# Kernel tuning notes

Measured on AMD Instinct MI355X. Metric: run time of the kernel, lower is better.

Reference implementation:

```python
import jax, jax.numpy as jnp
import numpy as np

DIM, HEAD, FFN = 256, 4, 1024
NEG = -1e9


def layer_norm(x, g, b, eps=1e-5):
    mu = jnp.mean(x, axis=-1, keepdims=True)
    var = jnp.mean((x - mu) ** 2, axis=-1, keepdims=True)
    return (x - mu) / jnp.sqrt(var + eps) * g + b


def setup_inputs() -> dict:
    key = jax.random.key(0)
    ks = jax.random.split(key, 10)
    B, T, D = 8, 2048, DIM
    s = 1.0 / np.sqrt(D)
    x = jax.random.normal(ks[0], (B, T, D), dtype=jnp.float32)
    mask = jax.random.randint(ks[1], (B, T), 0, 2).astype(jnp.float32)
    Wqkv = jax.random.uniform(ks[2], (3 * D, D), jnp.float32, -s, s)
    bqkv = jnp.zeros((3 * D,), jnp.float32)
    Wo = jax.random.uniform(ks[3], (D, D), jnp.float32, -s, s)
    bo = jnp.zeros((D,), jnp.float32)
    W1 = jax.random.uniform(ks[4], (FFN, D), jnp.float32, -s, s)
    b1 = jnp.zeros((FFN,), jnp.float32)
    W2 = jax.random.uniform(ks[5], (D, FFN), jnp.float32, -1.0 / np.sqrt(FFN), 1.0 / np.sqrt(FFN))
    b2 = jnp.zeros((D,), jnp.float32)
    g1 = jnp.ones((D,), jnp.float32); be1 = jnp.zeros((D,), jnp.float32)
    g2 = jnp.ones((D,), jnp.float32); be2 = jnp.zeros((D,), jnp.float32)
    return dict(x=x, mask=mask, Wqkv=Wqkv, bqkv=bqkv, Wo=Wo, bo=bo,
                W1=W1, b1=b1, W2=W2, b2=b2, g1=g1, be1=be1, g2=g2, be2=be2)


def _forward(x, mask, Wqkv, bqkv, Wo, bo, W1, b1, W2, b2, g1, be1, g2, be2):
    B, T, D = x.shape
    H = HEAD
    hd = D // H
    # --- MultiheadAttention (explicit, non-flash path, need_weights=True) ---
    qkv = jnp.einsum('btd,ed->bte', x, Wqkv) + bqkv            # (B,T,3D)
    q, k, v = jnp.split(qkv, 3, axis=-1)
    q = q.reshape(B, T, H, hd).transpose(0, 2, 1, 3)           # (B,H,T,hd)
    k = k.reshape(B, T, H, hd).transpose(0, 2, 1, 3)
    v = v.reshape(B, T, H, hd).transpose(0, 2, 1, 3)
    scores = jnp.einsum('bhqd,bhkd->bhqk', q, k) / jnp.sqrt(jnp.float32(hd))
    scores = jnp.where(mask[:, None, None, :] > 0.5, NEG, scores)
    w = jax.nn.softmax(scores, axis=-1)                        # (B,H,T,T)
    attn = jnp.einsum('bhqk,bhkd->bhqd', w, v)                 # (B,H,T,hd)
    attn = attn.transpose(0, 2, 1, 3).reshape(B, T, D)
    attn_out = jnp.einsum('btd,ed->bte', attn, Wo) + bo        # (B,T,D)
    w_avg = jnp.mean(w, axis=1)                                # (B,T,T), averaged over heads
    # halting score: sum over query dim (dim=1), then masked softmax
    halting = jnp.sum(w_avg, axis=1)                           # (B,T)
    halting = jax.nn.softmax(halting + mask * (-1e10), axis=-1)
    # --- residual + LN + FFN + LN ---
    h = layer_norm(x + attn_out, g1, be1)
    ffn = jnp.einsum('btf,df->btd', jax.nn.relu(jnp.einsum('btd,fd->btf', h, W1) + b1), W2) + b2
    out = layer_norm(h + ffn, g2, be2)
    return out, halting


def reference(x, mask, Wqkv, bqkv, Wo, bo, W1, b1, W2, b2, g1, be1, g2, be2):
    return _forward(x, mask, Wqkv, bqkv, Wo, bo, W1, b1, W2, b2, g1, be1, g2, be2)
```

## Files before the change

### kernel.cpp

```cpp
#include <hip/hip_runtime.h>
#include <hip/hip_bf16.h>
#include <math.h>

namespace {

constexpr int B = 8, T = 2048, D = 256, H = 4, HD = 64, FF = 1024;
constexpr float QSCALE = 0.18033688f;

typedef __attribute__((ext_vector_type(8))) short short8;
typedef __attribute__((ext_vector_type(4))) short s16x4;
typedef __attribute__((ext_vector_type(4))) float f32x4;

__device__ __forceinline__ short f2bf(float f) {
    __hip_bfloat16 h = __float2bfloat16(f);
    return *reinterpret_cast<short*>(&h);
}
__device__ __forceinline__ float bf2f(short s) {
    union { unsigned u; float f; } c;
    c.u = ((unsigned)(unsigned short)s) << 16;
    return c.f;
}
__device__ __forceinline__ float exp2a(float x) {
    float r; asm("v_exp_f32 %0, %1" : "=v"(r) : "v"(x)); return r;
}
__device__ __forceinline__ unsigned cvtpk(float lo, float hi) {
    unsigned r; asm("v_cvt_pk_bf16_f32 %0, %1, %2" : "=v"(r) : "v"(lo), "v"(hi)); return r;
}

__global__ __launch_bounds__(256) void k_cvt(
        const float* __restrict__ x,  const float* __restrict__ wq,
        const float* __restrict__ wo, const float* __restrict__ w1,
        const float* __restrict__ w2,
        short* __restrict__ x16,  short* __restrict__ wq16,
        short* __restrict__ wo16, short* __restrict__ w116,
        short* __restrict__ w216) {
    const int N0 = 524288, N1 = 24576, N2 = 8192, N3 = 32768, N4 = 32768;
    const int total = N0 + N1 + N2 + N3 + N4;
    for (int i = blockIdx.x*256 + threadIdx.x; i < total; i += gridDim.x*256) {
        const float* s; short* d; int j = i;
        if (j < N0) { s = x; d = x16; }
        else { j -= N0;
            if (j < N1) { s = wq; d = wq16; }
            else { j -= N1;
                if (j < N2) { s = wo; d = wo16; }
                else { j -= N2;
                    if (j < N3) { s = w1; d = w116; }
                    else { j -= N3; s = w2; d = w216; }
                }
            }
        }
        float4 a = ((const float4*)s)[j*2], b2 = ((const float4*)s)[j*2+1];
        short8 o;
        o[0]=f2bf(a.x);  o[1]=f2bf(a.y);  o[2]=f2bf(a.z);  o[3]=f2bf(a.w);
        o[4]=f2bf(b2.x); o[5]=f2bf(b2.y); o[6]=f2bf(b2.z); o[7]=f2bf(b2.w);
        ((short8*)d)[j] = o;
    }
}

template<int MODE>
__global__ __launch_bounds__(256) void k_gemm(
        const short* __restrict__ A, const short* __restrict__ W,
        const float* __restrict__ bias, const int K,
        short* __restrict__ oq, short* __restrict__ ok, short* __restrict__ ov,
        float* __restrict__ of, short* __restrict__ o16) {
    __shared__ short As[64][72];
    __shared__ short Ws[64][72];
    __shared__ float Cs[64][68];
    const int tid = threadIdx.x;
    const int w = tid >> 6, lane = tid & 63;
    const int qr = lane & 15, g = lane >> 4;
    const int wm = w >> 1, wn = w & 1;
    const int m0 = blockIdx.x * 64;
    const int n0 = blockIdx.y * 64;
    const int srow = tid >> 2, scol = (tid & 3) * 8;
    const short* Ag = A + (size_t)(m0 + srow) * K + scol;
    const short* Wg = W + (size_t)(n0 + srow) * K + scol;

    f32x4 acc[2][2];
    #pragma unroll
    for (int i = 0; i < 2; i++)
        #pragma unroll
        for (int j = 0; j < 2; j++) acc[i][j] = (f32x4){0.f, 0.f, 0.f, 0.f};

    for (int k0 = 0; k0 < K; k0 += 64) {
        __syncthreads();
        *(short8*)&As[srow][scol]      = *(const short8*)(Ag + k0);
        *(short8*)&As[srow][scol + 32] = *(const short8*)(Ag + k0 + 32);
        *(short8*)&Ws[srow][scol]      = *(const short8*)(Wg + k0);
        *(short8*)&Ws[srow][scol + 32] = *(const short8*)(Wg + k0 + 32);
        __syncthreads();
        #pragma unroll
        for (int kk = 0; kk < 2; kk++) {
            short8 a0 = *(const short8*)&As[wm*32 + qr][g*8 + kk*32];
            short8 a1 = *(const short8*)&As[wm*32 + 16 + qr][g*8 + kk*32];
            short8 b0 = *(const short8*)&Ws[wn*32 + qr][g*8 + kk*32];
            short8 b1 = *(const short8*)&Ws[wn*32 + 16 + qr][g*8 + kk*32];
            acc[0][0] = __builtin_amdgcn_mfma_f32_16x16x32_bf16(a0, b0, acc[0][0], 0, 0, 0);
            acc[0][1] = __builtin_amdgcn_mfma_f32_16x16x32_bf16(a0, b1, acc[0][1], 0, 0, 0);
            acc[1][0] = __builtin_amdgcn_mfma_f32_16x16x32_bf16(a1, b0, acc[1][0], 0, 0, 0);
            acc[1][1] = __builtin_amdgcn_mfma_f32_16x16x32_bf16(a1, b1, acc[1][1], 0, 0, 0);
        }
    }

    const int b = m0 >> 11;
    const int tl0 = m0 & (T - 1);

    if (MODE == 0 && blockIdx.y >= 8) {
        const int h = (int)blockIdx.y - 8;
        #pragma unroll
        for (int fm = 0; fm < 2; fm++) {
            const int tbase = tl0 + wm*32 + fm*16 + g*4;
            #pragma unroll
            for (int fn = 0; fn < 2; fn++) {
                const int d = wn*32 + fn*16 + qr;
                const float bv = bias[n0 + d];
                s16x4 pk;
                #pragma unroll
                for (int r = 0; r < 4; r++) pk[r] = f2bf(acc[fm][fn][r] + bv);
                *(s16x4*)&ov[((size_t)(b*H + h)*HD + d)*T + tbase] = pk;
            }
        }
        return;
    }

    #pragma unroll
    for (int fm = 0; fm < 2; fm++)
        #pragma unroll
        for (int fn = 0; fn < 2; fn++)
            #pragma unroll
            for (int r = 0; r < 4; r++)
                Cs[wm*32 + fm*16 + g*4 + r][wn*32 + fn*16 + qr] = acc[fm][fn][r];
    __syncthreads();
    const int row = tid >> 2, c0 = (tid & 3) * 16;
    float vals[16];
    #pragma unroll
    for (int j = 0; j < 16; j++) vals[j] = Cs[row][c0 + j] + bias[n0 + c0 + j];

    if (MODE == 0) {
        const int by = blockIdx.y;
        short* dst = (by < 4) ? oq : ok;
        const float qs = (by < 4) ? QSCALE : 1.0f;
        const int h = by & 3;
        short8 s0, s1;
        #pragma unroll
        for (int j = 0; j < 8; j++) { s0[j] = f2bf(vals[j]*qs); s1[j] = f2bf(vals[8+j]*qs); }
        short* p = dst + ((size_t)(b*H + h)*T + tl0 + row)*HD + c0;
        *(short8*)p = s0;
        *(short8*)(p + 8) = s1;
    } else if (MODE == 1 || MODE == 3) {
        float* p = of + (size_t)(m0 + row)*256 + n0 + c0;
        #pragma unroll
        for (int jj = 0; jj < 4; jj++) *(float4*)(p + jj*4) = *(float4*)&vals[jj*4];
    } else {
        short8 s0, s1;
        #pragma unroll
        for (int j = 0; j < 8; j++) {
            s0[j] = f2bf(fmaxf(vals[j], 0.f));
            s1[j] = f2bf(fmaxf(vals[8+j], 0.f));
        }
        short* p = o16 + (size_t)(m0 + row)*1024 + n0 + c0;
        *(short8*)p = s0;
        *(short8*)(p + 8) = s1;
    }
}

__global__ __launch_bounds__(256) void k_flash1(
        const short* __restrict__ qb, const short* __restrict__ kb,
        const short* __restrict__ vtb, const float* __restrict__ mask,
        short* __restrict__ opart, float* __restrict__ lpart) {
    __shared__ short Ks[64][72];
    __shared__ short Vt[64][72];
    __shared__ short Ps[4][16][72];
    __shared__ float mskb[64];

    const int tid = threadIdx.x;
    const int w = tid >> 6, lane = tid & 63;
    const int qr = lane & 15, g = lane >> 4;
    const int kh = blockIdx.x & 1, qt = blockIdx.x >> 1;
    const int h = blockIdx.y, b = blockIdx.z;
    const int bh = b*H + h;
    const int q0 = qt*64 + w*16;

    const short* qg = qb + ((size_t)bh * T + q0) * HD;
    const short8 qf0 = *(const short8*)(qg + qr*HD + g*8);
    const short8 qf1 = *(const short8*)(qg + qr*HD + 32 + g*8);

    const short* kg0 = kb + (size_t)bh * T * HD + (size_t)kh * 1024 * HD;
    const short* vg0 = vtb + (size_t)bh * HD * T + kh * 1024;
    const float* mg  = mask + (size_t)b * T + kh * 1024;
    const int skey = tid >> 2, sc = tid & 3;

    float lrun = 0.f;
    f32x4 oa[4];
    #pragma unroll
    for (int i = 0; i < 4; i++) oa[i] = (f32x4){0.f, 0.f, 0.f, 0.f};

    for (int kt = 0; kt < 16; kt++) {
        __syncthreads();
        {
            const short* kg = kg0 + (size_t)(kt*64) * HD;
            *(short8*)&Ks[skey][sc*8]      = *(const short8*)(kg + skey*HD + sc*8);
            *(short8*)&Ks[skey][sc*8 + 32] = *(const short8*)(kg + skey*HD + sc*8 + 32);
            const short* vg = vg0 + kt*64;
            *(short8*)&Vt[skey][sc*8]      = *(const short8*)(vg + (size_t)skey*T + sc*8);
            *(short8*)&Vt[skey][sc*8 + 32] = *(const short8*)(vg + (size_t)skey*T + sc*8 + 32);
            if (tid < 64) mskb[tid] = (mg[kt*64 + tid] > 0.5f) ? -1e9f : 0.f;
        }
        __syncthreads();

        float p[4][4];
        float lsum = 0.f;
        #pragma unroll
        for (int t4 = 0; t4 < 4; t4++) {
            const float4 mb4 = *(const float4*)&mskb[t4*16 + 4*g];
            f32x4 sa = (f32x4){mb4.x, mb4.y, mb4.z, mb4.w};
            short8 kf0 = *(const short8*)&Ks[t4*16 + qr][g*8];
            short8 kf1 = *(const short8*)&Ks[t4*16 + qr][g*8 + 32];
            sa = __builtin_amdgcn_mfma_f32_16x16x32_bf16(kf0, qf0, sa, 0, 0, 0);
            sa = __builtin_amdgcn_mfma_f32_16x16x32_bf16(kf1, qf1, sa, 0, 0, 0);
            p[t4][0] = exp2a(sa[0]);
            p[t4][1] = exp2a(sa[1]);
            p[t4][2] = exp2a(sa[2]);
            p[t4][3] = exp2a(sa[3]);
            lsum += (p[t4][0] + p[t4][1]) + (p[t4][2] + p[t4][3]);
        }
        lsum += __shfl_xor(lsum, 16, 64);
        lsum += __shfl_xor(lsum, 32, 64);
        lrun += lsum;

        #pragma unroll
        for (int t4 = 0; t4 < 4; t4++) {
            union { unsigned u[2]; s16x4 s; } cv;
            cv.u[0] = cvtpk(p[t4][0], p[t4][1]);
            cv.u[1] = cvtpk(p[t4][2], p[t4][3]);
            *(s16x4*)&Ps[w][qr][t4*16 + 4*g] = cv.s;
        }
        asm volatile("" ::: "memory");
        const short8 pa0 = *(const short8*)&Ps[w][qr][g*8];
        const short8 pa1 = *(const short8*)&Ps[w][qr][g*8 + 32];

        #pragma unroll
        for (int nt = 0; nt < 4; nt++) {
            short8 vf0 = *(const short8*)&Vt[nt*16 + qr][g*8];
            short8 vf1 = *(const short8*)&Vt[nt*16 + qr][g*8 + 32];
            oa[nt] = __builtin_amdgcn_mfma_f32_16x16x32_bf16(vf0, pa0, oa[nt], 0, 0, 0);
            oa[nt] = __builtin_amdgcn_mfma_f32_16x16x32_bf16(vf1, pa1, oa[nt], 0, 0, 0);
        }
    }

    const size_t obase = ((size_t)(kh*32 + bh)*2048 + q0 + qr) * 64;
    #pragma unroll
    for (int nt = 0; nt < 4; nt++) {
        s16x4 pk;
        #pragma unroll
        for (int r = 0; r < 4; r++) pk[r] = f2bf(oa[nt][r]);
        *(s16x4*)&opart[obase + nt*16 + 4*g] = pk;
    }
    if (lane < 16)
        lpart[(size_t)(kh*32 + bh)*2048 + q0 + qr] = lrun;
}

__global__ __launch_bounds__(256) void k_comb(
        const short* __restrict__ opart, const float* __restrict__ lpart,
        short* __restrict__ attnb, float* __restrict__ invlb) {
    const int j = blockIdx.x*256 + threadIdx.x;
    const size_t flat = (size_t)j * 8;
    const int d0 = (int)(flat & 63);
    const int q  = (int)((flat >> 6) & 2047);
    const int bh = (int)(flat >> 17);
    short8 o0 = *(const short8*)&opart[flat];
    short8 o1 = *(const short8*)&opart[flat + (size_t)4194304];
    const float l = lpart[bh*2048 + q] + lpart[65536 + bh*2048 + q];
    const float inv = 1.f / l;
    short8 r;
    #pragma unroll
    for (int i = 0; i < 8; i++) r[i] = f2bf((bf2f(o0[i]) + bf2f(o1[i])) * inv);
    const int b = bh >> 2, h = bh & 3;
    *(short8*)&attnb[((size_t)(b*2048 + q))*256 + h*64 + d0] = r;
    if (d0 == 0) invlb[bh*2048 + q] = inv;
}

__global__ __launch_bounds__(256) void k_flash2(
        const short* __restrict__ qb, const short* __restrict__ kb,
        const float* __restrict__ mask, const float* __restrict__ invlb,
        float* __restrict__ part) {
    __shared__ short Ks[64][72];
    __shared__ float mskb[64];
    __shared__ float colacc[4][64];

    const int tid = threadIdx.x;
    const int w = tid >> 6, lane = tid & 63;
    const int qr = lane & 15, g = lane >> 4;
    const int kh = blockIdx.x & 1, qt = blockIdx.x >> 1;
    const int h = blockIdx.y, b = blockIdx.z;
    const int bh = b*H + h;
    const int q0 = qt*64 + w*16;

    const short* qg = qb + ((size_t)bh * T + q0) * HD;
    const short8 qf0 = *(const short8*)(qg + qr*HD + g*8);
    const short8 qf1 = *(const short8*)(qg + qr*HD + 32 + g*8);

    float linv[4];
    #pragma unroll
    for (int r = 0; r < 4; r++) linv[r] = invlb[bh*2048 + q0 + 4*g + r];

    const short* kg0 = kb + (size_t)bh * T * HD + (size_t)kh * 1024 * HD;
    const float* mg  = mask + (size_t)b * T + kh * 1024;
    const int skey = tid >> 2, sc = tid & 3;

    for (int kt = 0; kt < 16; kt++) {
        __syncthreads();
        {
            const short* kg = kg0 + (size_t)(kt*64) * HD;
            *(short8*)&Ks[skey][sc*8]      = *(const short8*)(kg + skey*HD + sc*8);
            *(short8*)&Ks[skey][sc*8 + 32] = *(const short8*)(kg + skey*HD + sc*8 + 32);
            if (tid < 64) mskb[tid] = (mg[kt*64 + tid] > 0.5f) ? -1e9f : 0.f;
        }
        __syncthreads();
        float cs[4];
        #pragma unroll
        for (int t4 = 0; t4 < 4; t4++) {
            const float mb = mskb[t4*16 + qr];
            f32x4 sa = (f32x4){mb, mb, mb, mb};
            short8 kf0 = *(const short8*)&Ks[t4*16 + qr][g*8];
            short8 kf1 = *(const short8*)&Ks[t4*16 + qr][g*8 + 32];
            sa = __builtin_amdgcn_mfma_f32_16x16x32_bf16(qf0, kf0, sa, 0, 0, 0);
            sa = __builtin_amdgcn_mfma_f32_16x16x32_bf16(qf1, kf1, sa, 0, 0, 0);
            cs[t4] = exp2a(sa[0])*linv[0] + exp2a(sa[1])*linv[1]
                   + exp2a(sa[2])*linv[2] + exp2a(sa[3])*linv[3];
        }
        #pragma unroll
        for (int t4 = 0; t4 < 4; t4++) {
            cs[t4] += __shfl_xor(cs[t4], 16, 64);
            cs[t4] += __shfl_xor(cs[t4], 32, 64);
        }
        if (lane < 16) {
            #pragma unroll
            for (int t4 = 0; t4 < 4; t4++) colacc[w][t4*16 + lane] = cs[t4];
        }
        __syncthreads();
        if (tid < 64)
            part[((size_t)bh*32 + qt)*T + kh*1024 + kt*64 + tid] =
                colacc[0][tid] + colacc[1][tid] + colacc[2][tid] + colacc[3][tid];
    }
}

__global__ __launch_bounds__(256) void k_red(
        const float* __restrict__ part, float* __restrict__ red) {
    __shared__ float s[128];
    const int b = blockIdx.y, kc = blockIdx.x;
    const int tid = threadIdx.x;
    const int c = tid & 127, half = tid >> 7;
    const int k = kc*128 + c;
    const float* pb = part + ((size_t)(b*128 + half*64))*T + k;
    float acc = 0.f;
    #pragma unroll 8
    for (int r = 0; r < 64; r++) acc += pb[(size_t)r*T];
    if (half) s[c] = acc;
    __syncthreads();
    if (!half) red[(size_t)b*T + k] = acc + s[c];
}

__global__ __launch_bounds__(256) void k_halt(
        const float* __restrict__ red, const float* __restrict__ mask,
        float* __restrict__ outh) {
    __shared__ float redm[4], reds[4];
    const int b = blockIdx.x, tid = threadIdx.x;
    const float* mg = mask + (size_t)b * T;
    float v[8];
    float M = -3e38f;
    #pragma unroll
    for (int i = 0; i < 8; i++) {
        v[i] = red[(size_t)b*T + tid + i*256]*0.25f + mg[tid + i*256]*(-1e10f);
        M = fmaxf(M, v[i]);
    }
    #pragma unroll
    for (int off = 1; off < 64; off <<= 1) M = fmaxf(M, __shfl_xor(M, off, 64));
    const int wv = tid >> 6, lane = tid & 63;
    if (lane == 0) redm[wv] = M;
    __syncthreads();
    M = fmaxf(fmaxf(redm[0], redm[1]), fmaxf(redm[2], redm[3]));
    float S = 0.f;
    #pragma unroll
    for (int i = 0; i < 8; i++) { v[i] = __expf(v[i] - M); S += v[i]; }
    #pragma unroll
    for (int off = 1; off < 64; off <<= 1) S += __shfl_xor(S, off, 64);
    if (lane == 0) reds[wv] = S;
    __syncthreads();
    const float invS = 1.f / (reds[0] + reds[1] + reds[2] + reds[3]);
    #pragma unroll
    for (int i = 0; i < 8; i++) outh[(size_t)b*T + tid + i*256] = v[i]*invS;
}

__global__ __launch_bounds__(256) void k_ln(
        const float* __restrict__ a, const float* __restrict__ bsrc,
        const float* __restrict__ g, const float* __restrict__ be,
        float* __restrict__ yf, short* __restrict__ y16) {
    __shared__ float s[16][D];
    const int tid = threadIdx.x;
    const size_t row0 = (size_t)blockIdx.x * 16;
    const float4* ag = (const float4*)(a + row0*D);
    const float4* bg = (const float4*)(bsrc + row0*D);
    #pragma unroll
    for (int i = 0; i < 4; i++) {
        float4 av = ag[tid + i*256], bv = bg[tid + i*256];
        float4 sv = {av.x+bv.x, av.y+bv.y, av.z+bv.z, av.w+bv.w};
        ((float4*)&s[0][0])[tid + i*256] = sv;
    }
    __syncthreads();
    const int wv = tid >> 6, lane = tid & 63;
    float gvv[4], bvv[4];
    #pragma unroll
    for (int s2 = 0; s2 < 4; s2++) { gvv[s2] = g[lane + 64*s2]; bvv[s2] = be[lane + 64*s2]; }
    #pragma unroll
    for (int rr = 0; rr < 4; rr++) {
        const int r = wv*4 + rr;
        float x0 = s[r][lane],     x1 = s[r][lane+64];
        float x2 = s[r][lane+128], x3 = s[r][lane+192];
        float sum = x0+x1+x2+x3;
        float ssq = x0*x0 + x1*x1 + x2*x2 + x3*x3;
        #pragma unroll
        for (int off = 1; off < 64; off <<= 1) {
            sum += __shfl_xor(sum, off, 64);
            ssq += __shfl_xor(ssq, off, 64);
        }
        const float mu = sum * (1.f/256.f);
        const float rs = rsqrtf(ssq*(1.f/256.f) - mu*mu + 1e-5f);
        float y0 = (x0 - mu)*rs*gvv[0] + bvv[0];
        float y1 = (x1 - mu)*rs*gvv[1] + bvv[1];
        float y2 = (x2 - mu)*rs*gvv[2] + bvv[2];
        float y3 = (x3 - mu)*rs*gvv[3] + bvv[3];
        float* yp = yf + (row0 + r)*D;
        yp[lane]     = y0;
        yp[lane+64]  = y1;
        yp[lane+128] = y2;
        yp[lane+192] = y3;
        if (y16) {
            short* hp = y16 + (row0 + r)*D;
            hp[lane]     = f2bf(y0);
            hp[lane+64]  = f2bf(y1);
            hp[lane+128] = f2bf(y2);
            hp[lane+192] = f2bf(y3);
        }
    }
}

}

extern "C" void kernel_launch(void* const* d_in, const int* in_sizes, int n_in,
                              void* d_out, int out_size, void* d_ws, size_t ws_size,
                              hipStream_t stream) {
    (void)in_sizes; (void)n_in; (void)out_size; (void)ws_size;
    const float* x    = (const float*)d_in[0];
    const float* mask = (const float*)d_in[1];
    const float* Wqkv = (const float*)d_in[2];
    const float* bqkv = (const float*)d_in[3];
    const float* Wo   = (const float*)d_in[4];
    const float* bo   = (const float*)d_in[5];
    const float* W1   = (const float*)d_in[6];
    const float* b1   = (const float*)d_in[7];
    const float* W2   = (const float*)d_in[8];
    const float* b2   = (const float*)d_in[9];
    const float* g1   = (const float*)d_in[10];
    const float* be1  = (const float*)d_in[11];
    const float* g2   = (const float*)d_in[12];
    const float* be2  = (const float*)d_in[13];

    float* out  = (float*)d_out;
    char*  wsb  = (char*)d_ws;
    const size_t MB = 1024*1024;

    short* qb16   = (short*)(wsb + 0*MB);
    short* kb16   = (short*)(wsb + 8*MB);
    short* vt16   = (short*)(wsb + 16*MB);
    short* x16    = (short*)(wsb + 24*MB);
    short* attn16 = (short*)(wsb + 24*MB);
    short* opart  = (short*)(wsb + 32*MB);
    float* part   = (float*)(wsb + 32*MB);
    float* redb   = (float*)(wsb + 40*MB);
    float* hb     = (float*)(wsb + 48*MB);
    short* h16    = (short*)(wsb + 64*MB);
    float* lpart  = (float*)(wsb + 72*MB);
    float* invlb  = (float*)(wsb + 72*MB + 524288);
    short* wq16   = (short*)(wsb + 73*MB);
    short* wo16   = (short*)(wsb + 73*MB + 393216);
    short* w116   = (short*)(wsb + 73*MB + 524288);
    short* w216   = (short*)(wsb + 73*MB + 1048576);
    float* po     = (float*)(wsb + 75*MB);
    float* fo     = (float*)(wsb + 75*MB);
    short* mid16  = (short*)(wsb + 0*MB);
    float* outh   = out + (size_t)B*T*D;

    k_cvt    <<<dim3(1024),        256, 0, stream>>>(x, Wqkv, Wo, W1, W2,
                                                     x16, wq16, wo16, w116, w216);
    k_gemm<0><<<dim3(256, 12),     256, 0, stream>>>(x16, wq16, bqkv, 256,
                                                     qb16, kb16, vt16, nullptr, nullptr);
    k_flash1 <<<dim3(64, H, B),    256, 0, stream>>>(qb16, kb16, vt16, mask, opart, lpart);
    k_comb   <<<dim3(2048),        256, 0, stream>>>(opart, lpart, attn16, invlb);
    k_flash2 <<<dim3(64, H, B),    256, 0, stream>>>(qb16, kb16, mask, invlb, part);
    k_red    <<<dim3(16, B),       256, 0, stream>>>(part, redb);
    k_halt   <<<dim3(B),           256, 0, stream>>>(redb, mask, outh);
    k_gemm<1><<<dim3(256, 4),      256, 0, stream>>>(attn16, wo16, bo, 256,
                                                     nullptr, nullptr, nullptr, po, nullptr);
    k_ln     <<<dim3(B*T/16),      256, 0, stream>>>(x, po, g1, be1, hb, h16);
    k_gemm<2><<<dim3(256, 16),     256, 0, stream>>>(h16, w116, b1, 256,
                                                     nullptr, nullptr, nullptr, nullptr, mid16);
    k_gemm<3><<<dim3(256, 4),      256, 0, stream>>>(mid16, w216, b2, 1024,
                                                     nullptr, nullptr, nullptr, fo, nullptr);
    k_ln     <<<dim3(B*T/16),      256, 0, stream>>>(hb, fo, g2, be2, out, nullptr);
}
```

Before: 237.6 us.

## Precompute softmax log-normalizer, fuse PV with column sums, drop LDS staging

A new pass computes each query row's log-sum-exp normalizer up front. The PV kernel then produces already-normalized probabilities and accumulates per-key column sums for the halting score in the same pass, which removes the separate flash2 recompute and the normalization work in the combine kernel. The GEMM and flash kernels now read operands straight from global memory instead of staging them through LDS with barriers. In exchange, QK^T is still computed twice, the per-wave column-sum partials are much larger and make k_red read more data, and the direct global loads rely on the caches instead of LDS reuse.

After: 622.1 us. +161.8%, slower.

```diff
diff --git a/kernel.cpp b/kernel.cpp
--- a/kernel.cpp
+++ b/kernel.cpp
@@ -63,8 +63,6 @@
         const float* __restrict__ bias, const int K,
         short* __restrict__ oq, short* __restrict__ ok, short* __restrict__ ov,
         float* __restrict__ of, short* __restrict__ o16) {
-    __shared__ short As[64][72];
-    __shared__ short Ws[64][72];
     __shared__ float Cs[64][68];
     const int tid = threadIdx.x;
     const int w = tid >> 6, lane = tid & 63;
@@ -72,9 +70,11 @@
     const int wm = w >> 1, wn = w & 1;
     const int m0 = blockIdx.x * 64;
     const int n0 = blockIdx.y * 64;
-    const int srow = tid >> 2, scol = (tid & 3) * 8;
-    const short* Ag = A + (size_t)(m0 + srow) * K + scol;
-    const short* Wg = W + (size_t)(n0 + srow) * K + scol;
+
+    const short* Am0 = A + (size_t)(m0 + wm*32 + qr) * K + g*8;
+    const short* Am1 = A + (size_t)(m0 + wm*32 + 16 + qr) * K + g*8;
+    const short* Wn0 = W + (size_t)(n0 + wn*32 + qr) * K + g*8;
+    const short* Wn1 = W + (size_t)(n0 + wn*32 + 16 + qr) * K + g*8;
 
     f32x4 acc[2][2];
     #pragma unroll
@@ -83,18 +83,13 @@
         for (int j = 0; j < 2; j++) acc[i][j] = (f32x4){0.f, 0.f, 0.f, 0.f};
 
     for (int k0 = 0; k0 < K; k0 += 64) {
-        __syncthreads();
-        *(short8*)&As[srow][scol]      = *(const short8*)(Ag + k0);
-        *(short8*)&As[srow][scol + 32] = *(const short8*)(Ag + k0 + 32);
-        *(short8*)&Ws[srow][scol]      = *(const short8*)(Wg + k0);
-        *(short8*)&Ws[srow][scol + 32] = *(const short8*)(Wg + k0 + 32);
-        __syncthreads();
         #pragma unroll
         for (int kk = 0; kk < 2; kk++) {
-            short8 a0 = *(const short8*)&As[wm*32 + qr][g*8 + kk*32];
-            short8 a1 = *(const short8*)&As[wm*32 + 16 + qr][g*8 + kk*32];
-            short8 b0 = *(const short8*)&Ws[wn*32 + qr][g*8 + kk*32];
-            short8 b1 = *(const short8*)&Ws[wn*32 + 16 + qr][g*8 + kk*32];
+            const int off = k0 + kk*32;
+            short8 a0 = *(const short8*)(Am0 + off);
+            short8 a1 = *(const short8*)(Am1 + off);
+            short8 b0 = *(const short8*)(Wn0 + off);
+            short8 b1 = *(const short8*)(Wn1 + off);
             acc[0][0] = __builtin_amdgcn_mfma_f32_16x16x32_bf16(a0, b0, acc[0][0], 0, 0, 0);
             acc[0][1] = __builtin_amdgcn_mfma_f32_16x16x32_bf16(a0, b1, acc[0][1], 0, 0, 0);
             acc[1][0] = __builtin_amdgcn_mfma_f32_16x16x32_bf16(a1, b0, acc[1][0], 0, 0, 0);
@@ -164,14 +159,52 @@
     }
 }
 
-__global__ __launch_bounds__(256) void k_flash1(
+__global__ __launch_bounds__(256) void k_flashL(
+        const short* __restrict__ qb, const short* __restrict__ kb,
+        const float* __restrict__ mask, float* __restrict__ liout) {
+    const int tid = threadIdx.x;
+    const int w = tid >> 6, lane = tid & 63;
+    const int qr = lane & 15, g = lane >> 4;
+    const int qt = blockIdx.x, h = blockIdx.y, b = blockIdx.z;
+    const int bh = b*H + h;
+    const int q0 = qt*64 + w*16;
+
+    const short* qg = qb + ((size_t)bh * T + q0) * HD;
+    const short8 qf0 = *(const short8*)(qg + qr*HD + g*8);
+    const short8 qf1 = *(const short8*)(qg + qr*HD + 32 + g*8);
+    const short* kg0 = kb + (size_t)bh * T * HD + g*8;
+    const float* mg  = mask + (size_t)b * T;
+
+    float lrun = 0.f;
+    for (int kt = 0; kt < 32; kt++) {
+        #pragma unroll
+        for (int t4 = 0; t4 < 4; t4++) {
+            const int key0 = kt*64 + t4*16;
+            const float4 mv4 = *(const float4*)(mg + key0 + 4*g);
+            f32x4 sa = (f32x4){ (mv4.x > 0.5f) ? -1e9f : 0.f,
+                                (mv4.y > 0.5f) ? -1e9f : 0.f,
+                                (mv4.z > 0.5f) ? -1e9f : 0.f,
+                                (mv4.w > 0.5f) ? -1e9f : 0.f };
+            const short* kp = kg0 + (size_t)(key0 + qr) * HD;
+            short8 kf0 = *(const short8*)kp;
+            short8 kf1 = *(const short8*)(kp + 32);
+            sa = __builtin_amdgcn_mfma_f32_16x16x32_bf16(kf0, qf0, sa, 0, 0, 0);
+            sa = __builtin_amdgcn_mfma_f32_16x16x32_bf16(kf1, qf1, sa, 0, 0, 0);
+            lrun += (exp2a(sa[0]) + exp2a(sa[1])) + (exp2a(sa[2]) + exp2a(sa[3]));
+        }
+    }
+    lrun += __shfl_xor(lrun, 16, 64);
+    lrun += __shfl_xor(lrun, 32, 64);
+    if (g == 0)
+        liout[(size_t)bh*T + q0 + qr] = -__log2f(lrun);
+}
+
+__global__ __launch_bounds__(256) void k_flashPV(
         const short* __restrict__ qb, const short* __restrict__ kb,
         const short* __restrict__ vtb, const float* __restrict__ mask,
-        short* __restrict__ opart, float* __restrict__ lpart) {
-    __shared__ short Ks[64][72];
-    __shared__ short Vt[64][72];
-    __shared__ short Ps[4][16][72];
-    __shared__ float mskb[64];
+        const float* __restrict__ liout,
+        short* __restrict__ opart, float* __restrict__ part4) {
+    __shared__ short Ps[4][16][68];
 
     const int tid = threadIdx.x;
     const int w = tid >> 6, lane = tid & 63;
@@ -184,50 +217,38 @@
     const short* qg = qb + ((size_t)bh * T + q0) * HD;
     const short8 qf0 = *(const short8*)(qg + qr*HD + g*8);
     const short8 qf1 = *(const short8*)(qg + qr*HD + 32 + g*8);
-
-    const short* kg0 = kb + (size_t)bh * T * HD + (size_t)kh * 1024 * HD;
-    const short* vg0 = vtb + (size_t)bh * HD * T + kh * 1024;
-    const float* mg  = mask + (size_t)b * T + kh * 1024;
-    const int skey = tid >> 2, sc = tid & 3;
-
-    float lrun = 0.f;
+    const float li = liout[(size_t)bh*T + q0 + qr];
+
+    const short* kg0 = kb + (size_t)bh * T * HD + (size_t)kh*1024*HD + g*8;
+    const short* vg0 = vtb + (size_t)bh * HD * T + kh*1024;
+    const float* mg  = mask + (size_t)b * T + kh*1024;
+
     f32x4 oa[4];
     #pragma unroll
     for (int i = 0; i < 4; i++) oa[i] = (f32x4){0.f, 0.f, 0.f, 0.f};
 
+    float* prow = part4 + ((size_t)((bh*32 + qt)*4 + w))*T + kh*1024 + lane;
+
     for (int kt = 0; kt < 16; kt++) {
-        __syncthreads();
-        {
-            const short* kg = kg0 + (size_t)(kt*64) * HD;
-            *(short8*)&Ks[skey][sc*8]      = *(const short8*)(kg + skey*HD + sc*8);
-            *(short8*)&Ks[skey][sc*8 + 32] = *(const short8*)(kg + skey*HD + sc*8 + 32);
-            const short* vg = vg0 + kt*64;
-            *(short8*)&Vt[skey][sc*8]      = *(const short8*)(vg + (size_t)skey*T + sc*8);
-            *(short8*)&Vt[skey][sc*8 + 32] = *(const short8*)(vg + (size_t)skey*T + sc*8 + 32);
-            if (tid < 64) mskb[tid] = (mg[kt*64 + tid] > 0.5f) ? -1e9f : 0.f;
-        }
-        __syncthreads();
-
         float p[4][4];
-        float lsum = 0.f;
         #pragma unroll
         for (int t4 = 0; t4 < 4; t4++) {
-            const float4 mb4 = *(const float4*)&mskb[t4*16 + 4*g];
-            f32x4 sa = (f32x4){mb4.x, mb4.y, mb4.z, mb4.w};
-            short8 kf0 = *(const short8*)&Ks[t4*16 + qr][g*8];
-            short8 kf1 = *(const short8*)&Ks[t4*16 + qr][g*8 + 32];
+            const int key0 = kt*64 + t4*16;
+            const float4 mv4 = *(const float4*)(mg + key0 + 4*g);
+            f32x4 sa = (f32x4){ ((mv4.x > 0.5f) ? -1e9f : 0.f) + li,
+                                ((mv4.y > 0.5f) ? -1e9f : 0.f) + li,
+                                ((mv4.z > 0.5f) ? -1e9f : 0.f) + li,
+                                ((mv4.w > 0.5f) ? -1e9f : 0.f) + li };
+            const short* kp = kg0 + (size_t)(key0 + qr) * HD;
+            short8 kf0 = *(const short8*)kp;
+            short8 kf1 = *(const short8*)(kp + 32);
             sa = __builtin_amdgcn_mfma_f32_16x16x32_bf16(kf0, qf0, sa, 0, 0, 0);
             sa = __builtin_amdgcn_mfma_f32_16x16x32_bf16(kf1, qf1, sa, 0, 0, 0);
             p[t4][0] = exp2a(sa[0]);
             p[t4][1] = exp2a(sa[1]);
             p[t4][2] = exp2a(sa[2]);
             p[t4][3] = exp2a(sa[3]);
-            lsum += (p[t4][0] + p[t4][1]) + (p[t4][2] + p[t4][3]);
-        }
-        lsum += __shfl_xor(lsum, 16, 64);
-        lsum += __shfl_xor(lsum, 32, 64);
-        lrun += lsum;
-
+        }
         #pragma unroll
         for (int t4 = 0; t4 < 4; t4++) {
             union { unsigned u[2]; s16x4 s; } cv;
@@ -241,11 +262,16 @@
 
         #pragma unroll
         for (int nt = 0; nt < 4; nt++) {
-            short8 vf0 = *(const short8*)&Vt[nt*16 + qr][g*8];
-            short8 vf1 = *(const short8*)&Vt[nt*16 + qr][g*8 + 32];
+            const short* vp = vg0 + (size_t)(nt*16 + qr)*T + kt*64 + g*8;
+            short8 vf0 = *(const short8*)vp;
+            short8 vf1 = *(const short8*)(vp + 32);
             oa[nt] = __builtin_amdgcn_mfma_f32_16x16x32_bf16(vf0, pa0, oa[nt], 0, 0, 0);
             oa[nt] = __builtin_amdgcn_mfma_f32_16x16x32_bf16(vf1, pa1, oa[nt], 0, 0, 0);
         }
+        float cs = 0.f;
+        #pragma unroll
+        for (int q = 0; q < 16; q++) cs += bf2f(Ps[w][q][lane]);
+        prow[kt*64] = cs;
     }
 
     const size_t obase = ((size_t)(kh*32 + bh)*2048 + q0 + qr) * 64;
@@ -256,13 +282,10 @@
         for (int r = 0; r < 4; r++) pk[r] = f2bf(oa[nt][r]);
         *(s16x4*)&opart[obase + nt*16 + 4*g] = pk;
     }
-    if (lane < 16)
-        lpart[(size_t)(kh*32 + bh)*2048 + q0 + qr] = lrun;
 }
 
 __global__ __launch_bounds__(256) void k_comb(
-        const short* __restrict__ opart, const float* __restrict__ lpart,
-        short* __restrict__ attnb, float* __restrict__ invlb) {
+        const short* __restrict__ opart, short* __restrict__ attnb) {
     const int j = blockIdx.x*256 + threadIdx.x;
     const size_t flat = (size_t)j * 8;
     const int d0 = (int)(flat & 63);
@@ -270,92 +293,24 @@
     const int bh = (int)(flat >> 17);
     short8 o0 = *(const short8*)&opart[flat];
     short8 o1 = *(const short8*)&opart[flat + (size_t)4194304];
-    const float l = lpart[bh*2048 + q] + lpart[65536 + bh*2048 + q];
-    const float inv = 1.f / l;
     short8 r;
     #pragma unroll
-    for (int i = 0; i < 8; i++) r[i] = f2bf((bf2f(o0[i]) + bf2f(o1[i])) * inv);
+    for (int i = 0; i < 8; i++) r[i] = f2bf(bf2f(o0[i]) + bf2f(o1[i]));
     const int b = bh >> 2, h = bh & 3;
     *(short8*)&attnb[((size_t)(b*2048 + q))*256 + h*64 + d0] = r;
-    if (d0 == 0) invlb[bh*2048 + q] = inv;
-}
-
-__global__ __launch_bounds__(256) void k_flash2(
-        const short* __restrict__ qb, const short* __restrict__ kb,
-        const float* __restrict__ mask, const float* __restrict__ invlb,
-        float* __restrict__ part) {
-    __shared__ short Ks[64][72];
-    __shared__ float mskb[64];
-    __shared__ float colacc[4][64];
-
-    const int tid = threadIdx.x;
-    const int w = tid >> 6, lane = tid & 63;
-    const int qr = lane & 15, g = lane >> 4;
-    const int kh = blockIdx.x & 1, qt = blockIdx.x >> 1;
-    const int h = blockIdx.y, b = blockIdx.z;
-    const int bh = b*H + h;
-    const int q0 = qt*64 + w*16;
-
-    const short* qg = qb + ((size_t)bh * T + q0) * HD;
-    const short8 qf0 = *(const short8*)(qg + qr*HD + g*8);
-    const short8 qf1 = *(const short8*)(qg + qr*HD + 32 + g*8);
-
-    float linv[4];
-    #pragma unroll
-    for (int r = 0; r < 4; r++) linv[r] = invlb[bh*2048 + q0 + 4*g + r];
-
-    const short* kg0 = kb + (size_t)bh * T * HD + (size_t)kh * 1024 * HD;
-    const float* mg  = mask + (size_t)b * T + kh * 1024;
-    const int skey = tid >> 2, sc = tid & 3;
-
-    for (int kt = 0; kt < 16; kt++) {
-        __syncthreads();
-        {
-            const short* kg = kg0 + (size_t)(kt*64) * HD;
-            *(short8*)&Ks[skey][sc*8]      = *(const short8*)(kg + skey*HD + sc*8);
-            *(short8*)&Ks[skey][sc*8 + 32] = *(const short8*)(kg + skey*HD + sc*8 + 32);
-            if (tid < 64) mskb[tid] = (mg[kt*64 + tid] > 0.5f) ? -1e9f : 0.f;
-        }
-        __syncthreads();
-        float cs[4];
-        #pragma unroll
-        for (int t4 = 0; t4 < 4; t4++) {
-            const float mb = mskb[t4*16 + qr];
-            f32x4 sa = (f32x4){mb, mb, mb, mb};
-            short8 kf0 = *(const short8*)&Ks[t4*16 + qr][g*8];
-            short8 kf1 = *(const short8*)&Ks[t4*16 + qr][g*8 + 32];
-            sa = __builtin_amdgcn_mfma_f32_16x16x32_bf16(qf0, kf0, sa, 0, 0, 0);
-            sa = __builtin_amdgcn_mfma_f32_16x16x32_bf16(qf1, kf1, sa, 0, 0, 0);
-            cs[t4] = exp2a(sa[0])*linv[0] + exp2a(sa[1])*linv[1]
-                   + exp2a(sa[2])*linv[2] + exp2a(sa[3])*linv[3];
-        }
-        #pragma unroll
-        for (int t4 = 0; t4 < 4; t4++) {
-            cs[t4] += __shfl_xor(cs[t4], 16, 64);
-            cs[t4] += __shfl_xor(cs[t4], 32, 64);
-        }
-        if (lane < 16) {
-            #pragma unroll
-            for (int t4 = 0; t4 < 4; t4++) colacc[w][t4*16 + lane] = cs[t4];
-        }
-        __syncthreads();
-        if (tid < 64)
-            part[((size_t)bh*32 + qt)*T + kh*1024 + kt*64 + tid] =
-                colacc[0][tid] + colacc[1][tid] + colacc[2][tid] + colacc[3][tid];
-    }
 }
 
 __global__ __launch_bounds__(256) void k_red(
-        const float* __restrict__ part, float* __restrict__ red) {
+        const float* __restrict__ part4, float* __restrict__ red) {
     __shared__ float s[128];
     const int b = blockIdx.y, kc = blockIdx.x;
     const int tid = threadIdx.x;
     const int c = tid & 127, half = tid >> 7;
     const int k = kc*128 + c;
-    const float* pb = part + ((size_t)(b*128 + half*64))*T + k;
+    const float* pb = part4 + ((size_t)(b*512 + half*256))*T + k;
     float acc = 0.f;
     #pragma unroll 8
-    for (int r = 0; r < 64; r++) acc += pb[(size_t)r*T];
+    for (int r = 0; r < 256; r++) acc += pb[(size_t)r*T];
     if (half) s[c] = acc;
     __syncthreads();
     if (!half) red[(size_t)b*T + k] = acc + s[c];
@@ -475,30 +430,30 @@
     short* vt16   = (short*)(wsb + 16*MB);
     short* x16    = (short*)(wsb + 24*MB);
     short* attn16 = (short*)(wsb + 24*MB);
-    short* opart  = (short*)(wsb + 32*MB);
-    float* part   = (float*)(wsb + 32*MB);
-    float* redb   = (float*)(wsb + 40*MB);
-    float* hb     = (float*)(wsb + 48*MB);
-    short* h16    = (short*)(wsb + 64*MB);
-    float* lpart  = (float*)(wsb + 72*MB);
-    float* invlb  = (float*)(wsb + 72*MB + 524288);
-    short* wq16   = (short*)(wsb + 73*MB);
-    short* wo16   = (short*)(wsb + 73*MB + 393216);
-    short* w116   = (short*)(wsb + 73*MB + 524288);
-    short* w216   = (short*)(wsb + 73*MB + 1048576);
-    float* po     = (float*)(wsb + 75*MB);
-    float* fo     = (float*)(wsb + 75*MB);
-    short* mid16  = (short*)(wsb + 0*MB);
+    float* part4  = (float*)(wsb + 32*MB);
+    short* mid16  = (short*)(wsb + 32*MB);
+    short* opart  = (short*)(wsb + 64*MB);
+    float* hb     = (float*)(wsb + 64*MB);
+    short* h16    = (short*)(wsb + 80*MB);
+    float* liout  = (float*)(wsb + 88*MB);
+    float* redb   = (float*)(wsb + 88*MB + 262144);
+    short* wq16   = (short*)(wsb + 89*MB);
+    short* wo16   = (short*)(wsb + 89*MB + 393216);
+    short* w116   = (short*)(wsb + 89*MB + 524288);
+    short* w216   = (short*)(wsb + 89*MB + 1048576);
+    float* po     = (float*)(wsb + 0*MB);
+    float* fo     = (float*)(wsb + 0*MB);
     float* outh   = out + (size_t)B*T*D;
 
     k_cvt    <<<dim3(1024),        256, 0, stream>>>(x, Wqkv, Wo, W1, W2,
                                                      x16, wq16, wo16, w116, w216);
     k_gemm<0><<<dim3(256, 12),     256, 0, stream>>>(x16, wq16, bqkv, 256,
                                                      qb16, kb16, vt16, nullptr, nullptr);
-    k_flash1 <<<dim3(64, H, B),    256, 0, stream>>>(qb16, kb16, vt16, mask, opart, lpart);
-    k_comb   <<<dim3(2048),        256, 0, stream>>>(opart, lpart, attn16, invlb);
-    k_flash2 <<<dim3(64, H, B),    256, 0, stream>>>(qb16, kb16, mask, invlb, part);
-    k_red    <<<dim3(16, B),       256, 0, stream>>>(part, redb);
+    k_flashL <<<dim3(32, H, B),    256, 0, stream>>>(qb16, kb16, mask, liout);
+    k_flashPV<<<dim3(64, H, B),    256, 0, stream>>>(qb16, kb16, vt16, mask, liout,
+                                                     opart, part4);
+    k_comb   <<<dim3(2048),        256, 0, stream>>>(opart, attn16);
+    k_red    <<<dim3(16, B),       256, 0, stream>>>(part4, redb);
     k_halt   <<<dim3(B),           256, 0, stream>>>(redb, mask, outh);
     k_gemm<1><<<dim3(256, 4),      256, 0, stream>>>(attn16, wo16, bo, 256,
                                                      nullptr, nullptr, nullptr, po, nullptr);
```
